# Kernel optimization log

Measured on AMD Instinct MI355X. Metric: run time of the kernel, lower is better.

Reference implementation:

```python
import jax, jax.numpy as jnp
import numpy as np

TAGSET_BASE = 48            # original tag vocabulary
T = TAGSET_BASE + 2         # + START + STOP
START, STOP = TAGSET_BASE, TAGSET_BASE + 1
B, L = 1024, 512
NEG = -10000.0


def setup_inputs() -> dict:
    key = jax.random.key(0)
    k1, k2, k3, k4 = jax.random.split(key, 4)
    logits = jax.random.normal(k1, (B, L, T), dtype=jnp.float32)
    labels = jax.random.randint(k2, (B, L), 0, TAGSET_BASE)
    lens = jax.random.randint(k3, (B,), 1, L + 1)
    transitions = jax.random.normal(k4, (T, T), dtype=jnp.float32)
    transitions = transitions.at[START, :].set(NEG).at[:, STOP].set(NEG)
    return {"logits": logits, "transitions": transitions,
            "labels": labels, "lens": lens}


def reference(logits, transitions, labels, lens):
    """CRF negative log-likelihood: mean(partition - emission - transition)."""
    Bs, Ls, Ts = logits.shape
    start, stop = Ts - 2, Ts - 1

    # ---- forward algorithm (log-partition) via scan over time ----
    alpha0 = jnp.full((Bs, Ts), NEG, dtype=logits.dtype).at[:, start].set(0.0)

    def step(carry, logit_t):  # logit_t: [B, T]
        alpha, c = carry
        # mat[b,i,j] = trans[i,j] + alpha[b,j] + logit[b,i]
        mat = transitions[None, :, :] + alpha[:, None, :] + logit_t[:, :, None]
        alpha_nxt = jax.nn.logsumexp(mat, axis=2)
        alpha = jnp.where((c > 0)[:, None], alpha_nxt, alpha)
        return (alpha, c - 1), None

    (alpha, _), _ = jax.lax.scan(step, (alpha0, lens), jnp.swapaxes(logits, 0, 1))
    partition = jax.nn.logsumexp(alpha + transitions[stop][None, :], axis=1)  # [B]

    # ---- transition score of gold path ----
    labels_ext = jnp.concatenate([
        jnp.full((Bs, 1), start, dtype=labels.dtype),
        labels,
        jnp.full((Bs, 1), stop, dtype=labels.dtype)], axis=1)      # [B, L+2]
    pos = jnp.arange(Ls + 2)
    keep = pos[None, :] < (lens + 1)[:, None]
    labels_ext = jnp.where(keep, labels_ext, stop)
    # trans[next_tag, prev_tag]
    trn_scr = transitions[labels_ext[:, 1:], labels_ext[:, :-1]]   # [B, L+1]
    tmask = (jnp.arange(Ls + 1)[None, :] < (lens + 1)[:, None]).astype(logits.dtype)
    trans_score = jnp.sum(trn_scr * tmask, axis=1)                 # [B]

    # ---- emission score of gold path ----
    em = jnp.take_along_axis(logits, labels[:, :, None], axis=2)[:, :, 0]  # [B, L]
    emask = (jnp.arange(Ls)[None, :] < lens[:, None]).astype(logits.dtype)
    emission = jnp.sum(em * emask, axis=1)                         # [B]

    return jnp.sum(partition - emission - trans_score) / Bs
```

## Files before the change

### kernel.cpp

```cpp
#include <hip/hip_runtime.h>
#include <hip/hip_bf16.h>

#define TT 50
#define LL 512
#define BB 1024
#define START_TAG 48
#define STOP_TAG 49
#define RING 8
#define PFS 6
#define LN2F 0.69314718056f
#define UP_THR 0x1p40f
#define DN_THR 0x1p-20f

typedef __attribute__((ext_vector_type(4))) short bf16x4;
typedef __attribute__((ext_vector_type(4))) float f32x4;

typedef __attribute__((address_space(3))) unsigned int lds_u32_t;
typedef __attribute__((address_space(1))) const unsigned int glb_u32_t;

__device__ __forceinline__ void load_lds4(const void* g, void* l) {
    __builtin_amdgcn_global_load_lds((glb_u32_t*)g, (lds_u32_t*)l, 4, 0, 0);
}

__device__ __forceinline__ f32x4 mfma16(bf16x4 a, bf16x4 b, f32x4 c) {
#if __has_builtin(__builtin_amdgcn_mfma_f32_16x16x16bf16_1k)
    return __builtin_amdgcn_mfma_f32_16x16x16bf16_1k(a, b, c, 0, 0, 0);
#else
    f32x4 d;
    asm("v_mfma_f32_16x16x16_bf16 %0, %1, %2, %3\n\ts_nop 7\n\ts_nop 1"
        : "=v"(d) : "v"(a), "v"(b), "v"(c));
    return d;
#endif
}

__device__ __forceinline__ unsigned int cvtpk(float lo, float hi) {
    unsigned int w;
    asm("v_cvt_pk_bf16_f32 %0, %1, %2" : "=v"(w) : "v"(lo), "v"(hi));
    return w;
}
__device__ __forceinline__ bf16x4 bits_to_bf(unsigned int lo, unsigned int hi) {
    union { unsigned int u[2]; bf16x4 v; } c; c.u[0] = lo; c.u[1] = hi; return c.v;
}
__device__ __forceinline__ bf16x4 make_bf4(float a, float b, float c, float d) {
    return bits_to_bf(cvtpk(a, b), cvtpk(c, d));
}

template<bool BWD>
__device__ void run_chain(int g, int lane,
    const float* __restrict__ logits, const float* __restrict__ trans,
    const int* __restrict__ lens,
    float* __restrict__ vec_out, float* __restrict__ sc_out,
    float (&ring)[RING][12 * 64])
{
    const int col = lane & 15, grp = lane >> 4;
    const int b   = g * 16 + col;
    const int len = lens[b];
    const int mid = len >> 1;
    const int ns_eff = BWD ? (len - mid + 1) : mid;

    int km = ns_eff;
#pragma unroll
    for (int o = 1; o < 64; o <<= 1) km = max(km, __shfl_xor(km, o));

    bf16x4 A[3][3];
#pragma unroll
    for (int T = 0; T < 3; ++T)
#pragma unroll
        for (int C = 0; C < 3; ++C) {
            float v[4];
#pragma unroll
            for (int j = 0; j < 4; ++j) {
                const int m  = 16 * T + col;
                const int kk = 16 * C + 4 * grp + j;
                v[j] = __expf(BWD ? trans[kk * TT + m] : trans[m * TT + kk]);
            }
            A[T][C] = make_bf4(v[0], v[1], v[2], v[3]);
        }

    const int sseq = lane >> 2;
    const int sb   = g * 16 + sseq;
    const int slen = lens[sb];
    int soff[12], smin[12];
#pragma unroll
    for (int s = 0; s < 12; ++s) {
        const int stag  = 4 * s + (lane & 3);
        const int base0 = (sb * LL * TT + stag) * 4;
        smin[s] = base0;
        soff[s] = BWD ? base0 + (slen - 1) * TT * 4 : base0;
    }
    const char* gbase = (const char*)logits;

#pragma unroll
    for (int i = 0; i < PFS; ++i) {
#pragma unroll
        for (int s = 0; s < 12; ++s) {
            load_lds4(gbase + soff[s], &ring[i][s * 64]);
            soff[s] = BWD ? max(soff[s] - TT * 4, smin[s]) : soff[s] + TT * 4;
        }
    }
    asm volatile("s_waitcnt vmcnt(36)" ::: "memory");
    __builtin_amdgcn_sched_barrier(0);

    f32x4 l0a = *(const f32x4*)(&ring[0][(0 * 4 + grp) * 64 + col * 4]);
    f32x4 l0b = *(const f32x4*)(&ring[0][(1 * 4 + grp) * 64 + col * 4]);
    f32x4 l0c = *(const f32x4*)(&ring[0][(2 * 4 + grp) * 64 + col * 4]);
    unsigned int st[6];
#pragma unroll
    for (int C = 0; C < 3; ++C) {
        const f32x4 lg = (C == 0) ? l0a : (C == 1) ? l0b : l0c;
        float v[4];
#pragma unroll
        for (int j = 0; j < 4; ++j) {
            const int tag = 16 * C + 4 * grp + j;
            const float tv = BWD ? trans[STOP_TAG * TT + tag]
                                 : trans[tag * TT + START_TAG];
            v[j] = __expf(tv) * __expf(lg[j]);
        }
        st[2 * C]     = cvtpk(v[0], v[1]);
        st[2 * C + 1] = cvtpk(v[2], v[3]);
    }

    f32x4 e0, e1, e2;
    {
        f32x4 m0 = *(const f32x4*)(&ring[1][(0 * 4 + grp) * 64 + col * 4]);
        f32x4 m1 = *(const f32x4*)(&ring[1][(1 * 4 + grp) * 64 + col * 4]);
        f32x4 m2 = *(const f32x4*)(&ring[1][(2 * 4 + grp) * 64 + col * 4]);
#pragma unroll
        for (int j = 0; j < 4; ++j) { e0[j] = __expf(m0[j]); e1[j] = __expf(m1[j]); e2[j] = __expf(m2[j]); }
    }
    float shApp = 0.f, moff2 = 0.f;
    const f32x4 kZ = {0.f, 0.f, 0.f, 0.f};

    for (int k = 1; k < km; ++k) {
        asm volatile("s_waitcnt vmcnt(36)" ::: "memory");
        __builtin_amdgcn_sched_barrier(0);
        const float* sp = &ring[(k + 1) & (RING - 1)][0];
        f32x4 n0 = *(const f32x4*)(sp + (0 * 4 + grp) * 64 + col * 4);
        f32x4 n1 = *(const f32x4*)(sp + (1 * 4 + grp) * 64 + col * 4);
        f32x4 n2 = *(const f32x4*)(sp + (2 * 4 + grp) * 64 + col * 4);

        {
            float* dst = &ring[(k + PFS - 1) & (RING - 1)][0];
#pragma unroll
            for (int s = 0; s < 12; ++s) {
                load_lds4(gbase + soff[s], dst + s * 64);
                soff[s] = BWD ? max(soff[s] - TT * 4, smin[s]) : soff[s] + TT * 4;
            }
        }

        const bf16x4 B0 = bits_to_bf(st[0], st[1]);
        const bf16x4 B1 = bits_to_bf(st[2], st[3]);
        const bf16x4 B2 = bits_to_bf(st[4], st[5]);
        f32x4 a0 = mfma16(A[0][0], B0, kZ);
        f32x4 a1 = mfma16(A[1][0], B0, kZ);
        f32x4 a2 = mfma16(A[2][0], B0, kZ);
        a0 = mfma16(A[0][1], B1, a0);
        a1 = mfma16(A[1][1], B1, a1);
        a2 = mfma16(A[2][1], B1, a2);
        a0 = mfma16(A[0][2], B2, a0);
        a1 = mfma16(A[1][2], B2, a1);
        a2 = mfma16(A[2][2], B2, a2);

        const f32x4 p0 = a0 * e0, p1 = a1 * e1, p2 = a2 * e2;

        const bool live = (k < ns_eff);
        unsigned int w;
        w = cvtpk(p0.x, p0.y); st[0] = live ? w : st[0];
        w = cvtpk(p0.z, p0.w); st[1] = live ? w : st[1];
        w = cvtpk(p1.x, p1.y); st[2] = live ? w : st[2];
        w = cvtpk(p1.z, p1.w); st[3] = live ? w : st[3];
        w = cvtpk(p2.x, p2.y); st[4] = live ? w : st[4];
        w = cvtpk(p2.z, p2.w); st[5] = live ? w : st[5];
        moff2 = live ? (moff2 - shApp) : moff2;

        float sh = 0.f;
        if (k & 1) {
            float cm = fmaxf(fmaxf(fmaxf(p0.x, p0.y), fmaxf(p0.z, p0.w)),
                       fmaxf(fmaxf(fmaxf(p1.x, p1.y), fmaxf(p1.z, p1.w)),
                             fmaxf(fmaxf(p2.x, p2.y), fmaxf(p2.z, p2.w))));
            cm = fmaxf(cm, __shfl_xor(cm, 16));
            cm = fmaxf(cm, __shfl_xor(cm, 32));
            sh = (cm > UP_THR) ? -64.f : ((cm < DN_THR) ? 64.f : 0.f);
        }
#pragma unroll
        for (int j = 0; j < 4; ++j) {
            e0[j] = __expf(fmaf(sh, LN2F, n0[j]));
            e1[j] = __expf(fmaf(sh, LN2F, n1[j]));
            e2[j] = __expf(fmaf(sh, LN2F, n2[j]));
        }
        shApp = sh;
    }

    float fv[12];
#pragma unroll
    for (int C = 0; C < 3; ++C) {
        fv[4 * C + 0] = __uint_as_float(st[2 * C] << 16);
        fv[4 * C + 1] = __uint_as_float(st[2 * C] & 0xffff0000u);
        fv[4 * C + 2] = __uint_as_float(st[2 * C + 1] << 16);
        fv[4 * C + 3] = __uint_as_float(st[2 * C + 1] & 0xffff0000u);
    }
    float cm = fv[0];
#pragma unroll
    for (int i = 1; i < 12; ++i) cm = fmaxf(cm, fv[i]);
    cm = fmaxf(cm, __shfl_xor(cm, 16));
    cm = fmaxf(cm, __shfl_xor(cm, 32));
    const float r = 1.0f / cm;
#pragma unroll
    for (int C = 0; C < 3; ++C)
#pragma unroll
        for (int j = 0; j < 4; ++j)
            vec_out[(size_t)b * 64 + 16 * C + 4 * grp + j] = fv[4 * C + j] * r;
    if (grp == 0) sc_out[b] = moff2 * LN2F + logf(cm);
}

__global__ __launch_bounds__(128) void crf_chain(
    const float* __restrict__ logits, const float* __restrict__ trans,
    const int* __restrict__ labels, const int* __restrict__ lens,
    float* __restrict__ fvec, float* __restrict__ xvec,
    float* __restrict__ fs, float* __restrict__ bs,
    float* __restrict__ scp)
{
    __shared__ __align__(16) float ring[RING][12 * 64];
    const int g   = blockIdx.x >> 1;
    const int dir = blockIdx.x & 1;
    const int tid = threadIdx.x;
    if (tid < 64) {
        if (dir) run_chain<true >(g, tid, logits, trans, lens, xvec, bs, ring);
        else     run_chain<false>(g, tid, logits, trans, lens, fvec, fs, ring);
    } else {
        const int lane = tid - 64;
        const int seq = lane & 15, part = lane >> 4;
        const int b = g * 16 + seq;
        const int len = lens[b], mid = len >> 1;
        const int lo = dir ? mid : 0;
        const int hi = dir ? len : mid;
        float acc = 0.f;
        for (int t = lo + part; t < hi; t += 4) {
            const int lab = labels[b * LL + t];
            acc += logits[((size_t)(b * LL + t)) * TT + lab];
            const int prev = (t == 0) ? START_TAG : labels[b * LL + t - 1];
            acc += trans[lab * TT + prev];
            if (t == len - 1) acc += trans[STOP_TAG * TT + lab];
        }
        acc += __shfl_xor(acc, 16);
        acc += __shfl_xor(acc, 32);
        if (part == 0) scp[dir * BB + b] = acc;
    }
}

__global__ __launch_bounds__(64) void crf_combine(
    const float* __restrict__ logits, const float* __restrict__ trans,
    const int* __restrict__ lens,
    const float* __restrict__ fvec, const float* __restrict__ xvec,
    const float* __restrict__ fs, const float* __restrict__ bs,
    const float* __restrict__ scp, float* __restrict__ nll)
{
    const int b = blockIdx.x, lane = threadIdx.x;
    const int len = lens[b], mid = len >> 1;
    float part;
    if (len == 1) {
        float v = -3.0e38f;
        if (lane < TT)
            v = logits[(size_t)b * LL * TT + lane]
              + trans[lane * TT + START_TAG] + trans[STOP_TAG * TT + lane];
        float m = v;
#pragma unroll
        for (int o = 1; o < 64; o <<= 1) m = fmaxf(m, __shfl_xor(m, o));
        float s = __expf(v - m);
#pragma unroll
        for (int o = 1; o < 64; o <<= 1) s += __shfl_xor(s, o);
        part = m + logf(s);
    } else {
        float w = 0.f;
        if (lane < 48)
            w = fvec[(size_t)b * 64 + lane] * xvec[(size_t)b * 64 + lane]
              * __expf(-logits[((size_t)(b * LL + mid - 1)) * TT + lane]);
#pragma unroll
        for (int o = 1; o < 64; o <<= 1) w += __shfl_xor(w, o);
        part = logf(w) + fs[b] + bs[b];
    }
    if (lane == 0) nll[b] = part - scp[b] - scp[BB + b];
}

__global__ __launch_bounds__(1024) void crf_reduce(
    const float* __restrict__ nll, float* __restrict__ out)
{
    __shared__ float red[16];
    const int tid = threadIdx.x;
    float acc = nll[tid];
#pragma unroll
    for (int o = 32; o > 0; o >>= 1) acc += __shfl_xor(acc, o);
    if ((tid & 63) == 0) red[tid >> 6] = acc;
    __syncthreads();
    if (tid == 0) {
        float tot = 0.0f;
        for (int i = 0; i < 16; ++i) tot += red[i];
        out[0] = tot / (float)BB;
    }
}

extern "C" void kernel_launch(void* const* d_in, const int* in_sizes, int n_in,
                              void* d_out, int out_size, void* d_ws, size_t ws_size,
                              hipStream_t stream) {
    const float* logits = (const float*)d_in[0];
    const float* trans  = (const float*)d_in[1];
    const int*   labels = (const int*)d_in[2];
    const int*   lens   = (const int*)d_in[3];

    float* fvec = (float*)d_ws;
    float* xvec = fvec + BB * 64;
    float* fs   = xvec + BB * 64;
    float* bs   = fs + BB;
    float* scp  = bs + BB;
    float* nll  = scp + 2 * BB;
    float* out  = (float*)d_out;

    crf_chain<<<128, 128, 0, stream>>>(logits, trans, labels, lens,
                                       fvec, xvec, fs, bs, scp);
    crf_combine<<<BB, 64, 0, stream>>>(logits, trans, lens,
                                       fvec, xvec, fs, bs, scp, nll);
    crf_reduce<<<1, 1024, 0, stream>>>(nll, out);
}
```

Measured before the change: 134.6 us.

## Deepen prefetch, split MFMA accumulation chains, and delay rescale shift by one step

Raises the prefetch depth from 6 to 7 ring slots, with matching vmcnt waits. It splits each three-deep dependent MFMA accumulation chain into independent MFMAs that are summed with vector adds, which shortens MFMA latency on the serial recurrence. The renormalisation shift found at step k is now applied at step k+1, so the max-reduction and shuffles leave the critical path before the exp of the next emissions. The cost is more MFMA issues and extra adds, and the delayed shift allows one more step of possible overflow or underflow before rescaling.

```diff
diff --git a/kernel.cpp b/kernel.cpp
--- a/kernel.cpp
+++ b/kernel.cpp
@@ -7,7 +7,7 @@
 #define START_TAG 48
 #define STOP_TAG 49
 #define RING 8
-#define PFS 6
+#define PFS 7
 #define LN2F 0.69314718056f
 #define UP_THR 0x1p40f
 #define DN_THR 0x1p-20f
@@ -98,7 +98,7 @@
             soff[s] = BWD ? max(soff[s] - TT * 4, smin[s]) : soff[s] + TT * 4;
         }
     }
-    asm volatile("s_waitcnt vmcnt(36)" ::: "memory");
+    asm volatile("s_waitcnt vmcnt(60)" ::: "memory");
     __builtin_amdgcn_sched_barrier(0);
 
     f32x4 l0a = *(const f32x4*)(&ring[0][(0 * 4 + grp) * 64 + col * 4]);
@@ -128,11 +128,13 @@
 #pragma unroll
         for (int j = 0; j < 4; ++j) { e0[j] = __expf(m0[j]); e1[j] = __expf(m1[j]); e2[j] = __expf(m2[j]); }
     }
-    float shApp = 0.f, moff2 = 0.f;
+    float shApp = 0.f;
+    float shPend = 0.f;
+    float moff2 = 0.f;
     const f32x4 kZ = {0.f, 0.f, 0.f, 0.f};
 
     for (int k = 1; k < km; ++k) {
-        asm volatile("s_waitcnt vmcnt(36)" ::: "memory");
+        asm volatile("s_waitcnt vmcnt(48)" ::: "memory");
         __builtin_amdgcn_sched_barrier(0);
         const float* sp = &ring[(k + 1) & (RING - 1)][0];
         f32x4 n0 = *(const f32x4*)(sp + (0 * 4 + grp) * 64 + col * 4);
@@ -151,15 +153,18 @@
         const bf16x4 B0 = bits_to_bf(st[0], st[1]);
         const bf16x4 B1 = bits_to_bf(st[2], st[3]);
         const bf16x4 B2 = bits_to_bf(st[4], st[5]);
-        f32x4 a0 = mfma16(A[0][0], B0, kZ);
-        f32x4 a1 = mfma16(A[1][0], B0, kZ);
-        f32x4 a2 = mfma16(A[2][0], B0, kZ);
-        a0 = mfma16(A[0][1], B1, a0);
-        a1 = mfma16(A[1][1], B1, a1);
-        a2 = mfma16(A[2][1], B1, a2);
-        a0 = mfma16(A[0][2], B2, a0);
-        a1 = mfma16(A[1][2], B2, a1);
-        a2 = mfma16(A[2][2], B2, a2);
+        f32x4 a00 = mfma16(A[0][0], B0, kZ);
+        f32x4 a10 = mfma16(A[1][0], B0, kZ);
+        f32x4 a20 = mfma16(A[2][0], B0, kZ);
+        f32x4 a01 = mfma16(A[0][1], B1, kZ);
+        f32x4 a11 = mfma16(A[1][1], B1, kZ);
+        f32x4 a21 = mfma16(A[2][1], B1, kZ);
+        f32x4 a02 = mfma16(A[0][2], B2, kZ);
+        f32x4 a12 = mfma16(A[1][2], B2, kZ);
+        f32x4 a22 = mfma16(A[2][2], B2, kZ);
+        const f32x4 a0 = (a00 + a01) + a02;
+        const f32x4 a1 = (a10 + a11) + a12;
+        const f32x4 a2 = (a20 + a21) + a22;
 
         const f32x4 p0 = a0 * e0, p1 = a1 * e1, p2 = a2 * e2;
 
@@ -173,22 +178,23 @@
         w = cvtpk(p2.z, p2.w); st[5] = live ? w : st[5];
         moff2 = live ? (moff2 - shApp) : moff2;
 
-        float sh = 0.f;
+        const float shUse = shPend;
+        shPend = 0.f;
         if (k & 1) {
             float cm = fmaxf(fmaxf(fmaxf(p0.x, p0.y), fmaxf(p0.z, p0.w)),
                        fmaxf(fmaxf(fmaxf(p1.x, p1.y), fmaxf(p1.z, p1.w)),
-                             fmaxf(fmaxf(p2.x, p2.y), fmaxf(p2.z, p2.w))));
+                             fmaxf(fmaxf(fmaxf(p2.x, p2.y), fmaxf(p2.z, p2.w)), 0.f)));
             cm = fmaxf(cm, __shfl_xor(cm, 16));
             cm = fmaxf(cm, __shfl_xor(cm, 32));
-            sh = (cm > UP_THR) ? -64.f : ((cm < DN_THR) ? 64.f : 0.f);
+            shPend = (cm > UP_THR) ? -64.f : ((cm < DN_THR) ? 64.f : 0.f);
         }
 #pragma unroll
         for (int j = 0; j < 4; ++j) {
-            e0[j] = __expf(fmaf(sh, LN2F, n0[j]));
-            e1[j] = __expf(fmaf(sh, LN2F, n1[j]));
-            e2[j] = __expf(fmaf(sh, LN2F, n2[j]));
-        }
-        shApp = sh;
+            e0[j] = __expf(fmaf(shUse, LN2F, n0[j]));
+            e1[j] = __expf(fmaf(shUse, LN2F, n1[j]));
+            e2[j] = __expf(fmaf(shUse, LN2F, n2[j]));
+        }
+        shApp = shUse;
     }
 
     float fv[12];
```

Measured after the change: 151.4 us. 12.5% more time.
